# Kernel optimization log

Measured on AMD Instinct MI355X. Metric: run time of the kernel, lower is better.

## Reference

```python
import jax, jax.numpy as jnp
import numpy as np

B, N, D = 2048, 64, 256
DH = D // 2  # theta/phi projection dim
EPS = 1e-5

def layer_norm(x, g, b):
    m = jnp.mean(x, axis=-1, keepdims=True)
    v = jnp.var(x, axis=-1, keepdims=True)
    return (x - m) * jax.lax.rsqrt(v + EPS) * g + b

def graph_conv(x, adj, th_w, ph_w, fc_w, fc_b):
    # static adjacency: softmax over rows, shared across batch
    A_static = jax.nn.softmax(adj, axis=-1)  # [N, N]
    q = jnp.einsum('bnd,hd->bnh', x, th_w)   # [B, N, DH]
    k = jnp.einsum('bnd,hd->bnh', x, ph_w)   # [B, N, DH]
    scores = jnp.einsum('bni,bmi->bnm', q, k) / jnp.sqrt(jnp.asarray(DH, x.dtype))
    A_hat = A_static[None] + jax.nn.softmax(scores, axis=-1)  # [B, N, N]
    agg = jnp.einsum('bnm,bmd->bnd', A_hat, x)
    return jnp.einsum('bnd,od->bno', agg, fc_w) + fc_b

def setup_inputs() -> dict:
    key = jax.random.key(0)
    ks = jax.random.split(key, 12)
    eye = jnp.eye(N, dtype=jnp.float32)
    s = 1.0 / np.sqrt(D)
    return {
        'graph':  jax.random.normal(ks[0], (B, N, D), jnp.float32),
        'ln_in_g': jnp.ones((D,), jnp.float32), 'ln_in_b': jnp.zeros((D,), jnp.float32),
        'adj0':  eye + 0.01 * jax.random.normal(ks[1], (N, N), jnp.float32),
        'th0':   jax.random.uniform(ks[2], (DH, D), jnp.float32, -s, s),
        'ph0':   jax.random.uniform(ks[3], (DH, D), jnp.float32, -s, s),
        'fcw0':  jax.random.uniform(ks[4], (D, D), jnp.float32, -s, s),
        'fcb0':  jax.random.uniform(ks[5], (D,), jnp.float32, -s, s),
        'ln0_g': jnp.ones((D,), jnp.float32), 'ln0_b': jnp.zeros((D,), jnp.float32),
        'adj1':  eye + 0.01 * jax.random.normal(ks[6], (N, N), jnp.float32),
        'th1':   jax.random.uniform(ks[7], (DH, D), jnp.float32, -s, s),
        'ph1':   jax.random.uniform(ks[8], (DH, D), jnp.float32, -s, s),
        'fcw1':  jax.random.uniform(ks[9], (D, D), jnp.float32, -s, s),
        'fcb1':  jax.random.uniform(ks[10], (D,), jnp.float32, -s, s),
    }

def reference(graph, ln_in_g, ln_in_b, adj0, th0, ph0, fcw0, fcb0,
              ln0_g, ln0_b, adj1, th1, ph1, fcw1, fcb1):
    x = layer_norm(graph, ln_in_g, ln_in_b)
    x = graph_conv(x, adj0, th0, ph0, fcw0, fcb0)
    x = layer_norm(x, ln0_g, ln0_b)
    x = jnp.where(x >= 0, x, 0.1 * x)  # LeakyReLU(0.1); dropout is identity in eval
    x = graph_conv(x, adj1, th1, ph1, fcw1, fcb1)
    return x
```

## Files before the change

### kernel.cpp

```cpp
#include <hip/hip_runtime.h>

typedef __bf16 bf16x8 __attribute__((ext_vector_type(8)));
typedef __bf16 bf16x4 __attribute__((ext_vector_type(4)));
typedef float  f32x4  __attribute__((ext_vector_type(4)));

constexpr int WS_AS0 = 0;
constexpr int WS_AS1 = 4096;
constexpr int WS_MT0 = 8192;
constexpr int WS_MT1 = 73728;
constexpr int WS_FC0 = 139264;
constexpr int WS_FC1 = 204800;

static __device__ __forceinline__ f32x4 mfma16(bf16x8 a, bf16x8 b, f32x4 c) {
    return __builtin_amdgcn_mfma_f32_16x16x32_bf16(a, b, c, 0, 0, 0);
}

__global__ void prep_adj(const float* __restrict__ adj0,
                         const float* __restrict__ adj1,
                         __bf16* __restrict__ wsb) {
    const int t = threadIdx.x;
    const int l = t >> 6, r = t & 63;
    const float* a = (l ? adj1 : adj0) + r * 64;
    float mx = -3.0e38f;
    for (int c = 0; c < 64; ++c) mx = fmaxf(mx, a[c]);
    float s = 0.f;
    for (int c = 0; c < 64; ++c) s += __expf(a[c] - mx);
    const float inv = 1.f / s;
    __bf16* dst = wsb + (l ? WS_AS1 : WS_AS0) + r * 64;
    for (int c = 0; c < 64; ++c) dst[c] = (__bf16)(__expf(a[c] - mx) * inv);
}

__global__ void prep_M(const float* __restrict__ th0, const float* __restrict__ ph0,
                       const float* __restrict__ th1, const float* __restrict__ ph1,
                       __bf16* __restrict__ wsb) {
    const int e = blockIdx.x & 255, layer = blockIdx.x >> 8, d = threadIdx.x;
    const float* th = layer ? th1 : th0;
    const float* ph = layer ? ph1 : ph0;
    float s = 0.f;
    for (int h = 0; h < 128; ++h) s += ph[h * 256 + e] * th[h * 256 + d];
    wsb[(layer ? WS_MT1 : WS_MT0) + e * 256 + d] = (__bf16)(s * 0.088388347648318447f);
}

__global__ void prep_w(const float* __restrict__ fc0, const float* __restrict__ fc1,
                       __bf16* __restrict__ wsb) {
    int i = blockIdx.x * 256 + threadIdx.x;
    if (i >= 131072) return;
    if (i < 65536) wsb[WS_FC0 + i] = (__bf16)fc0[i];
    else           wsb[WS_FC1 + i - 65536] = (__bf16)fc1[i - 65536];
}

__global__ __launch_bounds__(512, 4) void fused_gcn(
    const float* __restrict__ graph,
    const float* __restrict__ ln_in_g, const float* __restrict__ ln_in_b,
    const __bf16* __restrict__ wsb,
    const float* __restrict__ fcb0, const float* __restrict__ ln0_g,
    const float* __restrict__ ln0_b, const float* __restrict__ fcb1,
    float* __restrict__ outp)
{
    constexpr int XN_S = 264;
    constexpr int ZT_S = 72;
    constexpr int AH_S = 72;

    __shared__ __align__(16) __bf16 sXn[64 * XN_S];
    __shared__ __align__(16) __bf16 sR1[256 * ZT_S];
    __shared__ __align__(16) __bf16 sAh[64 * AH_S];
    __shared__ float sRed[128];

    const int tid = threadIdx.x;
    const int w = tid >> 6, lane = tid & 63;
    const int l15 = lane & 15, qd = lane >> 4;
    const int b = blockIdx.x;

    {
        if (tid < 128) sRed[tid] = 0.f;
        const int r = tid >> 3, ci = (tid & 7) * 32;
        const float* gp = graph + (size_t)b * 16384 + r * 256 + ci;
        f32x4 v[8];
        float s = 0.f, s2 = 0.f;
        #pragma unroll
        for (int j = 0; j < 8; ++j) {
            v[j] = *(const f32x4*)(gp + j * 4);
            #pragma unroll
            for (int e = 0; e < 4; ++e) { s += v[j][e]; s2 += v[j][e] * v[j][e]; }
        }
        #pragma unroll
        for (int m = 1; m <= 4; m <<= 1) { s += __shfl_xor(s, m); s2 += __shfl_xor(s2, m); }
        const float mean = s * (1.f / 256.f);
        const float var  = s2 * (1.f / 256.f) - mean * mean;
        const float rstd = rsqrtf(var + 1e-5f);
        #pragma unroll
        for (int j = 0; j < 8; ++j) {
            f32x4 gg = *(const f32x4*)(ln_in_g + ci + j * 4);
            f32x4 bb = *(const f32x4*)(ln_in_b + ci + j * 4);
            bf16x4 pk;
            #pragma unroll
            for (int e = 0; e < 4; ++e)
                pk[e] = (__bf16)((v[j][e] - mean) * rstd * gg[e] + bb[e]);
            *(bf16x4*)&sXn[r * XN_S + ci + j * 4] = pk;
        }
    }
    __syncthreads();

    #pragma unroll
    for (int layer = 0; layer < 2; ++layer) {
        const __bf16* As  = wsb + (layer ? WS_AS1 : WS_AS0);
        const __bf16* mtw = wsb + (layer ? WS_MT1 : WS_MT0);
        const __bf16* fcw = wsb + (layer ? WS_FC1 : WS_FC0);
        const float*  fcb = layer ? fcb1 : fcb0;

        {
            f32x4 tacc[2][4];
            #pragma unroll
            for (int jm = 0; jm < 2; ++jm)
                #pragma unroll
                for (int nt = 0; nt < 4; ++nt) tacc[jm][nt] = (f32x4){0.f, 0.f, 0.f, 0.f};
            #pragma unroll
            for (int kk = 0; kk < 8; ++kk) {
                bf16x8 a0 = *(const bf16x8*)(mtw + ((w * 2 + 0) * 16 + l15) * 256 + kk * 32 + qd * 8);
                bf16x8 a1 = *(const bf16x8*)(mtw + ((w * 2 + 1) * 16 + l15) * 256 + kk * 32 + qd * 8);
                #pragma unroll
                for (int nt = 0; nt < 4; ++nt) {
                    bf16x8 bx = *(const bf16x8*)&sXn[(nt * 16 + l15) * XN_S + kk * 32 + qd * 8];
                    tacc[0][nt] = mfma16(a0, bx, tacc[0][nt]);
                    tacc[1][nt] = mfma16(a1, bx, tacc[1][nt]);
                }
            }
            #pragma unroll
            for (int jm = 0; jm < 2; ++jm)
                #pragma unroll
                for (int nt = 0; nt < 4; ++nt) {
                    bf16x4 pk;
                    #pragma unroll
                    for (int r = 0; r < 4; ++r) pk[r] = (__bf16)tacc[jm][nt][r];
                    *(bf16x4*)&sR1[(nt * 16 + l15) * XN_S + (w * 2 + jm) * 16 + qd * 4] = pk;
                }
        }
        __syncthreads();

        bf16x4 zpk[8];
        if (w < 4) {
            const int mb = w * 16;
            bf16x8 at[8];
            #pragma unroll
            for (int kk = 0; kk < 8; ++kk)
                at[kk] = *(const bf16x8*)&sR1[(mb + l15) * XN_S + kk * 32 + qd * 8];
            f32x4 sc[4];
            #pragma unroll
            for (int nt = 0; nt < 4; ++nt) sc[nt] = (f32x4){0.f, 0.f, 0.f, 0.f};
            #pragma unroll
            for (int nt = 0; nt < 4; ++nt)
                #pragma unroll
                for (int kk = 0; kk < 8; ++kk) {
                    bf16x8 bx = *(const bf16x8*)&sXn[(nt * 16 + l15) * XN_S + kk * 32 + qd * 8];
                    sc[nt] = mfma16(at[kk], bx, sc[nt]);
                }
            #pragma unroll
            for (int r = 0; r < 4; ++r) {
                float v[4];
                #pragma unroll
                for (int nt = 0; nt < 4; ++nt) v[nt] = sc[nt][r];
                float mx = fmaxf(fmaxf(v[0], v[1]), fmaxf(v[2], v[3]));
                #pragma unroll
                for (int m = 1; m <= 8; m <<= 1) mx = fmaxf(mx, __shfl_xor(mx, m));
                float e[4], sum = 0.f;
                #pragma unroll
                for (int nt = 0; nt < 4; ++nt) { e[nt] = __expf(v[nt] - mx); sum += e[nt]; }
                #pragma unroll
                for (int m = 1; m <= 8; m <<= 1) sum += __shfl_xor(sum, m);
                const float inv = 1.f / sum;
                const int row = mb + qd * 4 + r;
                #pragma unroll
                for (int nt = 0; nt < 4; ++nt) {
                    const int col = nt * 16 + l15;
                    sAh[row * AH_S + col] = (__bf16)(e[nt] * inv + (float)As[row * 64 + col]);
                }
            }
        } else {
            const int ob = 128 + (w - 4) * 32;
            #pragma unroll
            for (int jm = 0; jm < 2; ++jm) {
                bf16x8 bfc[8];
                #pragma unroll
                for (int kk = 0; kk < 8; ++kk)
                    bfc[kk] = *(const bf16x8*)(fcw + (ob + jm * 16 + l15) * 256 + kk * 32 + qd * 8);
                #pragma unroll
                for (int m = 0; m < 4; ++m) {
                    f32x4 az = {0.f, 0.f, 0.f, 0.f};
                    #pragma unroll
                    for (int kk = 0; kk < 8; ++kk) {
                        bf16x8 ax = *(const bf16x8*)&sXn[(m * 16 + l15) * XN_S + kk * 32 + qd * 8];
                        az = mfma16(ax, bfc[kk], az);
                    }
                    bf16x4 pk;
                    #pragma unroll
                    for (int r = 0; r < 4; ++r) pk[r] = (__bf16)az[r];
                    zpk[jm * 4 + m] = pk;
                }
            }
        }
        __syncthreads();

        {
            if (w >= 4) {
                const int ob = 128 + (w - 4) * 32;
                #pragma unroll
                for (int jm = 0; jm < 2; ++jm)
                    #pragma unroll
                    for (int m = 0; m < 4; ++m)
                        *(bf16x4*)&sR1[(ob + jm * 16 + l15) * ZT_S + m * 16 + qd * 4] = zpk[jm * 4 + m];
            }
            const int o = w * 16 + l15;
            bf16x8 bfc[8];
            #pragma unroll
            for (int kk = 0; kk < 8; ++kk)
                bfc[kk] = *(const bf16x8*)(fcw + o * 256 + kk * 32 + qd * 8);
            #pragma unroll
            for (int m = 0; m < 4; ++m) {
                f32x4 az = {0.f, 0.f, 0.f, 0.f};
                #pragma unroll
                for (int kk = 0; kk < 8; ++kk) {
                    bf16x8 ax = *(const bf16x8*)&sXn[(m * 16 + l15) * XN_S + kk * 32 + qd * 8];
                    az = mfma16(ax, bfc[kk], az);
                }
                bf16x4 pk;
                #pragma unroll
                for (int r = 0; r < 4; ++r) pk[r] = (__bf16)az[r];
                *(bf16x4*)&sR1[o * ZT_S + m * 16 + qd * 4] = pk;
            }
        }
        __syncthreads();

        {
            const int mb = (w & 3) * 16, ng = w >> 2;
            bf16x8 aa[2];
            #pragma unroll
            for (int kk = 0; kk < 2; ++kk)
                aa[kk] = *(const bf16x8*)&sAh[(mb + l15) * AH_S + kk * 32 + qd * 8];
            f32x4 oacc[8];
            #pragma unroll
            for (int j = 0; j < 8; ++j) {
                const int o = ng * 128 + j * 16 + l15;
                f32x4 acc = {0.f, 0.f, 0.f, 0.f};
                #pragma unroll
                for (int kk = 0; kk < 2; ++kk) {
                    bf16x8 bb = *(const bf16x8*)&sR1[o * ZT_S + kk * 32 + qd * 8];
                    acc = mfma16(aa[kk], bb, acc);
                }
                const float bias = fcb[o];
                #pragma unroll
                for (int r = 0; r < 4; ++r) acc[r] += bias;
                oacc[j] = acc;
            }

            if (layer == 0) {
                #pragma unroll
                for (int r = 0; r < 4; ++r) {
                    float s = 0.f, s2 = 0.f;
                    #pragma unroll
                    for (int j = 0; j < 8; ++j) { const float vv = oacc[j][r]; s += vv; s2 += vv * vv; }
                    #pragma unroll
                    for (int m = 1; m <= 8; m <<= 1) { s += __shfl_xor(s, m); s2 += __shfl_xor(s2, m); }
                    if (l15 == 0) {
                        const int row = mb + qd * 4 + r;
                        atomicAdd(&sRed[row], s);
                        atomicAdd(&sRed[64 + row], s2);
                    }
                }
                __syncthreads();
                float mean4[4], rstd4[4];
                #pragma unroll
                for (int r = 0; r < 4; ++r) {
                    const int row = mb + qd * 4 + r;
                    const float mean = sRed[row] * (1.f / 256.f);
                    const float var  = sRed[64 + row] * (1.f / 256.f) - mean * mean;
                    mean4[r] = mean;
                    rstd4[r] = rsqrtf(var + 1e-5f);
                }
                #pragma unroll
                for (int j = 0; j < 8; ++j) {
                    const int o = ng * 128 + j * 16 + l15;
                    const float g = ln0_g[o], bb = ln0_b[o];
                    #pragma unroll
                    for (int r = 0; r < 4; ++r) {
                        float y = (oacc[j][r] - mean4[r]) * rstd4[r] * g + bb;
                        y = (y >= 0.f) ? y : 0.1f * y;
                        sXn[(mb + qd * 4 + r) * XN_S + o] = (__bf16)y;
                    }
                }
                __syncthreads();
            } else {
                float* op = outp + (size_t)b * 16384;
                #pragma unroll
                for (int j = 0; j < 8; ++j) {
                    const int o = ng * 128 + j * 16 + l15;
                    #pragma unroll
                    for (int r = 0; r < 4; ++r)
                        op[(mb + qd * 4 + r) * 256 + o] = oacc[j][r];
                }
            }
        }
    }
}

extern "C" void kernel_launch(void* const* d_in, const int* in_sizes, int n_in,
                              void* d_out, int out_size, void* d_ws, size_t ws_size,
                              hipStream_t stream) {
    const float* graph   = (const float*)d_in[0];
    const float* ln_in_g = (const float*)d_in[1];
    const float* ln_in_b = (const float*)d_in[2];
    const float* adj0    = (const float*)d_in[3];
    const float* th0     = (const float*)d_in[4];
    const float* ph0     = (const float*)d_in[5];
    const float* fcw0    = (const float*)d_in[6];
    const float* fcb0    = (const float*)d_in[7];
    const float* ln0_g   = (const float*)d_in[8];
    const float* ln0_b   = (const float*)d_in[9];
    const float* adj1    = (const float*)d_in[10];
    const float* th1     = (const float*)d_in[11];
    const float* ph1     = (const float*)d_in[12];
    const float* fcw1    = (const float*)d_in[13];
    const float* fcb1    = (const float*)d_in[14];
    __bf16* wsb = (__bf16*)d_ws;

    prep_adj<<<1, 128, 0, stream>>>(adj0, adj1, wsb);
    prep_M<<<512, 256, 0, stream>>>(th0, ph0, th1, ph1, wsb);
    prep_w<<<512, 256, 0, stream>>>(fcw0, fcw1, wsb);
    fused_gcn<<<2048, 512, 0, stream>>>(graph, ln_in_g, ln_in_b, wsb,
                                        fcb0, ln0_g, ln0_b, fcb1, (float*)d_out);
}
```

Baseline: 439.6 us.

## Merge prep kernels into one launch and restructure fused layer phases

Folds the three weight-prep kernels into a single prep_all launch and parallelises the adjacency softmax with wave shuffles, cutting launch overhead and a serial single-block kernel. Inside fused_gcn the layer loop is no longer unrolled. The static adjacency is staged into shared memory. The Z = X·fc^T product is now computed by all 8 waves in a separate phase after the softmax, where before half the waves overlapped it with the softmax through register staging. This adds a barrier and removes the overlap, in exchange for less register pressure and smaller code.

```diff
diff --git a/kernel.cpp b/kernel.cpp
--- a/kernel.cpp
+++ b/kernel.cpp
@@ -15,38 +15,43 @@
     return __builtin_amdgcn_mfma_f32_16x16x32_bf16(a, b, c, 0, 0, 0);
 }
 
-__global__ void prep_adj(const float* __restrict__ adj0,
-                         const float* __restrict__ adj1,
+__global__ void prep_all(const float* __restrict__ adj0, const float* __restrict__ adj1,
+                         const float* __restrict__ th0,  const float* __restrict__ ph0,
+                         const float* __restrict__ th1,  const float* __restrict__ ph1,
+                         const float* __restrict__ fc0,  const float* __restrict__ fc1,
                          __bf16* __restrict__ wsb) {
-    const int t = threadIdx.x;
-    const int l = t >> 6, r = t & 63;
-    const float* a = (l ? adj1 : adj0) + r * 64;
-    float mx = -3.0e38f;
-    for (int c = 0; c < 64; ++c) mx = fmaxf(mx, a[c]);
-    float s = 0.f;
-    for (int c = 0; c < 64; ++c) s += __expf(a[c] - mx);
-    const float inv = 1.f / s;
-    __bf16* dst = wsb + (l ? WS_AS1 : WS_AS0) + r * 64;
-    for (int c = 0; c < 64; ++c) dst[c] = (__bf16)(__expf(a[c] - mx) * inv);
-}
-
-__global__ void prep_M(const float* __restrict__ th0, const float* __restrict__ ph0,
-                       const float* __restrict__ th1, const float* __restrict__ ph1,
-                       __bf16* __restrict__ wsb) {
-    const int e = blockIdx.x & 255, layer = blockIdx.x >> 8, d = threadIdx.x;
-    const float* th = layer ? th1 : th0;
-    const float* ph = layer ? ph1 : ph0;
-    float s = 0.f;
-    for (int h = 0; h < 128; ++h) s += ph[h * 256 + e] * th[h * 256 + d];
-    wsb[(layer ? WS_MT1 : WS_MT0) + e * 256 + d] = (__bf16)(s * 0.088388347648318447f);
-}
-
-__global__ void prep_w(const float* __restrict__ fc0, const float* __restrict__ fc1,
-                       __bf16* __restrict__ wsb) {
-    int i = blockIdx.x * 256 + threadIdx.x;
-    if (i >= 131072) return;
-    if (i < 65536) wsb[WS_FC0 + i] = (__bf16)fc0[i];
-    else           wsb[WS_FC1 + i - 65536] = (__bf16)fc1[i - 65536];
+    const int blk = blockIdx.x, tid = threadIdx.x;
+    if (blk < 32) {
+        const int w = tid >> 6, lane = tid & 63;
+        const int row = blk * 4 + w;
+        const int layer = row >> 6, r = row & 63;
+        const float* a = (layer ? adj1 : adj0) + r * 64;
+        const float v = a[lane];
+        float mx = v;
+        #pragma unroll
+        for (int m = 1; m < 64; m <<= 1) mx = fmaxf(mx, __shfl_xor(mx, m));
+        float e = __expf(v - mx), sum = e;
+        #pragma unroll
+        for (int m = 1; m < 64; m <<= 1) sum += __shfl_xor(sum, m);
+        wsb[(layer ? WS_AS1 : WS_AS0) + r * 64 + lane] = (__bf16)(e / sum);
+    } else if (blk < 544) {
+        const int e = (blk - 32) & 255, layer = (blk - 32) >> 8, d = tid;
+        const float* th = layer ? th1 : th0;
+        const float* ph = layer ? ph1 : ph0;
+        float s = 0.f;
+        #pragma unroll 8
+        for (int h = 0; h < 128; ++h) s += ph[h * 256 + e] * th[h * 256 + d];
+        wsb[(layer ? WS_MT1 : WS_MT0) + e * 256 + d] = (__bf16)(s * 0.088388347648318447f);
+    } else {
+        const int i = (blk - 544) * 512 + tid * 2;
+        if (i < 65536) {
+            wsb[WS_FC0 + i]     = (__bf16)fc0[i];
+            wsb[WS_FC0 + i + 1] = (__bf16)fc0[i + 1];
+        } else {
+            wsb[WS_FC1 + i - 65536] = (__bf16)fc1[i - 65536];
+            wsb[WS_FC1 + i - 65535] = (__bf16)fc1[i - 65535];
+        }
+    }
 }
 
 __global__ __launch_bounds__(512, 4) void fused_gcn(
@@ -101,7 +106,7 @@
     }
     __syncthreads();
 
-    #pragma unroll
+    #pragma unroll 1
     for (int layer = 0; layer < 2; ++layer) {
         const __bf16* As  = wsb + (layer ? WS_AS1 : WS_AS0);
         const __bf16* mtw = wsb + (layer ? WS_MT1 : WS_MT0);
@@ -109,35 +114,37 @@
         const float*  fcb = layer ? fcb1 : fcb0;
 
         {
-            f32x4 tacc[2][4];
-            #pragma unroll
-            for (int jm = 0; jm < 2; ++jm)
-                #pragma unroll
-                for (int nt = 0; nt < 4; ++nt) tacc[jm][nt] = (f32x4){0.f, 0.f, 0.f, 0.f};
-            #pragma unroll
-            for (int kk = 0; kk < 8; ++kk) {
-                bf16x8 a0 = *(const bf16x8*)(mtw + ((w * 2 + 0) * 16 + l15) * 256 + kk * 32 + qd * 8);
-                bf16x8 a1 = *(const bf16x8*)(mtw + ((w * 2 + 1) * 16 + l15) * 256 + kk * 32 + qd * 8);
-                #pragma unroll
-                for (int nt = 0; nt < 4; ++nt) {
-                    bf16x8 bx = *(const bf16x8*)&sXn[(nt * 16 + l15) * XN_S + kk * 32 + qd * 8];
-                    tacc[0][nt] = mfma16(a0, bx, tacc[0][nt]);
-                    tacc[1][nt] = mfma16(a1, bx, tacc[1][nt]);
-                }
-            }
-            #pragma unroll
-            for (int jm = 0; jm < 2; ++jm)
+            {
+                const int r = tid >> 3, c8 = (tid & 7) * 8;
+                *(bf16x8*)&sAh[r * AH_S + c8] = *(const bf16x8*)(As + r * 64 + c8);
+            }
+            #pragma unroll
+            for (int jm = 0; jm < 2; ++jm) {
+                bf16x8 amt[8];
+                #pragma unroll
+                for (int kk = 0; kk < 8; ++kk)
+                    amt[kk] = *(const bf16x8*)(mtw + ((w * 2 + jm) * 16 + l15) * 256 + kk * 32 + qd * 8);
+                f32x4 tacc[4];
+                #pragma unroll
+                for (int nt = 0; nt < 4; ++nt) tacc[nt] = (f32x4){0.f, 0.f, 0.f, 0.f};
+                #pragma unroll
+                for (int kk = 0; kk < 8; ++kk)
+                    #pragma unroll
+                    for (int nt = 0; nt < 4; ++nt) {
+                        bf16x8 bx = *(const bf16x8*)&sXn[(nt * 16 + l15) * XN_S + kk * 32 + qd * 8];
+                        tacc[nt] = mfma16(amt[kk], bx, tacc[nt]);
+                    }
                 #pragma unroll
                 for (int nt = 0; nt < 4; ++nt) {
                     bf16x4 pk;
                     #pragma unroll
-                    for (int r = 0; r < 4; ++r) pk[r] = (__bf16)tacc[jm][nt][r];
+                    for (int r = 0; r < 4; ++r) pk[r] = (__bf16)tacc[nt][r];
                     *(bf16x4*)&sR1[(nt * 16 + l15) * XN_S + (w * 2 + jm) * 16 + qd * 4] = pk;
                 }
+            }
         }
         __syncthreads();
 
-        bf16x4 zpk[8];
         if (w < 4) {
             const int mb = w * 16;
             bf16x8 at[8];
@@ -172,60 +179,38 @@
                 #pragma unroll
                 for (int nt = 0; nt < 4; ++nt) {
                     const int col = nt * 16 + l15;
-                    sAh[row * AH_S + col] = (__bf16)(e[nt] * inv + (float)As[row * 64 + col]);
-                }
-            }
-        } else {
-            const int ob = 128 + (w - 4) * 32;
+                    const float as = (float)sAh[row * AH_S + col];
+                    sAh[row * AH_S + col] = (__bf16)(e[nt] * inv + as);
+                }
+            }
+        }
+        __syncthreads();
+
+        {
             #pragma unroll
             for (int jm = 0; jm < 2; ++jm) {
+                const int o = w * 32 + jm * 16 + l15;
                 bf16x8 bfc[8];
                 #pragma unroll
                 for (int kk = 0; kk < 8; ++kk)
-                    bfc[kk] = *(const bf16x8*)(fcw + (ob + jm * 16 + l15) * 256 + kk * 32 + qd * 8);
+                    bfc[kk] = *(const bf16x8*)(fcw + o * 256 + kk * 32 + qd * 8);
+                f32x4 zacc[4];
+                #pragma unroll
+                for (int m = 0; m < 4; ++m) zacc[m] = (f32x4){0.f, 0.f, 0.f, 0.f};
+                #pragma unroll
+                for (int kk = 0; kk < 8; ++kk)
+                    #pragma unroll
+                    for (int m = 0; m < 4; ++m) {
+                        bf16x8 ax = *(const bf16x8*)&sXn[(m * 16 + l15) * XN_S + kk * 32 + qd * 8];
+                        zacc[m] = mfma16(ax, bfc[kk], zacc[m]);
+                    }
                 #pragma unroll
                 for (int m = 0; m < 4; ++m) {
-                    f32x4 az = {0.f, 0.f, 0.f, 0.f};
-                    #pragma unroll
-                    for (int kk = 0; kk < 8; ++kk) {
-                        bf16x8 ax = *(const bf16x8*)&sXn[(m * 16 + l15) * XN_S + kk * 32 + qd * 8];
-                        az = mfma16(ax, bfc[kk], az);
-                    }
                     bf16x4 pk;
                     #pragma unroll
-                    for (int r = 0; r < 4; ++r) pk[r] = (__bf16)az[r];
-                    zpk[jm * 4 + m] = pk;
-                }
-            }
-        }
-        __syncthreads();
-
-        {
-            if (w >= 4) {
-                const int ob = 128 + (w - 4) * 32;
-                #pragma unroll
-                for (int jm = 0; jm < 2; ++jm)
-                    #pragma unroll
-                    for (int m = 0; m < 4; ++m)
-                        *(bf16x4*)&sR1[(ob + jm * 16 + l15) * ZT_S + m * 16 + qd * 4] = zpk[jm * 4 + m];
-            }
-            const int o = w * 16 + l15;
-            bf16x8 bfc[8];
-            #pragma unroll
-            for (int kk = 0; kk < 8; ++kk)
-                bfc[kk] = *(const bf16x8*)(fcw + o * 256 + kk * 32 + qd * 8);
-            #pragma unroll
-            for (int m = 0; m < 4; ++m) {
-                f32x4 az = {0.f, 0.f, 0.f, 0.f};
-                #pragma unroll
-                for (int kk = 0; kk < 8; ++kk) {
-                    bf16x8 ax = *(const bf16x8*)&sXn[(m * 16 + l15) * XN_S + kk * 32 + qd * 8];
-                    az = mfma16(ax, bfc[kk], az);
-                }
-                bf16x4 pk;
-                #pragma unroll
-                for (int r = 0; r < 4; ++r) pk[r] = (__bf16)az[r];
-                *(bf16x4*)&sR1[o * ZT_S + m * 16 + qd * 4] = pk;
+                    for (int r = 0; r < 4; ++r) pk[r] = (__bf16)zacc[m][r];
+                    *(bf16x4*)&sR1[o * ZT_S + m * 16 + qd * 4] = pk;
+                }
             }
         }
         __syncthreads();
@@ -322,9 +307,7 @@
     const float* fcb1    = (const float*)d_in[14];
     __bf16* wsb = (__bf16*)d_ws;
 
-    prep_adj<<<1, 128, 0, stream>>>(adj0, adj1, wsb);
-    prep_M<<<512, 256, 0, stream>>>(th0, ph0, th1, ph1, wsb);
-    prep_w<<<512, 256, 0, stream>>>(fcw0, fcw1, wsb);
+    prep_all<<<800, 256, 0, stream>>>(adj0, adj1, th0, ph0, th1, ph1, fcw0, fcw1, wsb);
     fused_gcn<<<2048, 512, 0, stream>>>(graph, ln_in_g, ln_in_b, wsb,
                                         fcb0, ln0_g, ln0_b, fcb1, (float*)d_out);
 }
```

Result: faster. 405.5 us (-7.8%).
